# Kernel optimization log

Measured on AMD Instinct MI355X. Metric: run time of the kernel, lower is better.

Reference implementation:

```python
import jax, jax.numpy as jnp
import numpy as np

D_MODEL = 1024
N_HEADS = 16
D_HEAD = D_MODEL // N_HEADS
EPS = 1e-6


def _phi(x):
    # elu(x) + 1, guaranteed non-negative kernel feature map
    return jax.nn.elu(x) + 1.0


def setup_inputs() -> dict:
    key = jax.random.key(0)
    k1, k2, k3 = jax.random.split(key, 3)
    x = jax.random.normal(k1, (4, 4096, D_MODEL), dtype=jnp.float32)
    # torch nn.Linear weights: (out_features, in_features), y = x @ W.T
    s = 1.0 / np.sqrt(D_MODEL)
    w_qkv = jax.random.uniform(k2, (3 * D_MODEL, D_MODEL), minval=-s, maxval=s, dtype=jnp.float32)
    w_out = jax.random.uniform(k3, (D_MODEL, D_MODEL), minval=-s, maxval=s, dtype=jnp.float32)
    return {"x": x, "w_qkv": w_qkv, "w_out": w_out}


def reference(x, w_qkv, w_out):
    B, L, D = x.shape
    H, dh = N_HEADS, D_HEAD
    qkv = jnp.einsum('bld,ed->ble', x, w_qkv)            # (B,L,3D)
    qkv = qkv.reshape(B, L, 3, H, dh).transpose(2, 0, 3, 1, 4)  # (3,B,H,L,dh)
    q, k, v = _phi(qkv[0]), _phi(qkv[1]), qkv[2]         # each (B,H,L,dh)

    # time-major for scan: (L,B,H,dh)
    qT = q.transpose(2, 0, 1, 3)
    kT = k.transpose(2, 0, 1, 3)
    vT = v.transpose(2, 0, 1, 3)

    S0 = jnp.zeros((B, H, dh, dh), dtype=x.dtype)
    z0 = jnp.zeros((B, H, dh), dtype=x.dtype)

    def step(carry, inp):
        S, z = carry
        q_t, k_t, v_t = inp
        S = S + k_t[..., :, None] * v_t[..., None, :]    # bhde outer product
        z = z + k_t
        num = jnp.einsum('bhde,bhd->bhe', S, q_t)
        den = jnp.maximum(jnp.sum(z * q_t, axis=-1, keepdims=True), EPS)
        return (S, z), num / den

    _, out = jax.lax.scan(step, (S0, z0), (qT, kT, vT))  # out: (L,B,H,dh)
    out = out.transpose(1, 0, 2, 3).reshape(B, L, D)     # (B,L,D)
    return jnp.einsum('bld,ed->ble', out, w_out)
```

## Files before the change

### kernel.cpp

```cpp
#include <hip/hip_runtime.h>
#include <hip/hip_bf16.h>
#include <math.h>

#define B_SZc    4
#define L_SEQc   4096
#define EPSc     1e-6f
#define CHUNKc   128
#define NCHUNKc  32

#define QKV_PER_B  4194304ull
#define ATT_PER_B  4194304ull
#define X_PER_B    4194304ull
#define S_PER_B    2097152ull
#define Z_PER_B    32768ull

typedef __attribute__((ext_vector_type(8))) short s16x8;
typedef __attribute__((ext_vector_type(4))) short s16x4;
typedef __attribute__((ext_vector_type(4))) float f32x4;

__device__ __forceinline__ float phi_f(float x) {
    return x > 0.0f ? x + 1.0f : expf(x);
}
__device__ __forceinline__ float bf2f(short h) {
    return __uint_as_float(((unsigned int)(unsigned short)h) << 16);
}
__device__ __forceinline__ short f2bf(float f) {
    unsigned int u = __float_as_uint(f);
    u = (u + 0x7FFFu + ((u >> 16) & 1u)) >> 16;
    return (short)u;
}

#define GLOAD16(ldsp, gp) \
    __builtin_amdgcn_global_load_lds((const __attribute__((address_space(1))) void*)(gp), \
                                     (__attribute__((address_space(3))) void*)(ldsp), 16, 0, 0)

__global__ __launch_bounds__(256)
void cvt_f32_bf16(const float* __restrict__ in, short* __restrict__ out, int n)
{
    int i = (blockIdx.x * 256 + threadIdx.x) * 4;
    const int stride = gridDim.x * 256 * 4;
    for (; i < n; i += stride) {
        float4 v = *(const float4*)(in + i);
        short4 o = {f2bf(v.x), f2bf(v.y), f2bf(v.z), f2bf(v.w)};
        *(short4*)(out + i) = o;
    }
}

template<int MODE>
__global__ __launch_bounds__(256)
void gemm_bf16(const short* __restrict__ A, const short* __restrict__ Bm,
               int M, int N, int K, float* __restrict__ C,
               short* __restrict__ qb, short* __restrict__ kb,
               short* __restrict__ kTb, short* __restrict__ vTb)
{
    __shared__ __align__(16) short lA[128 * 32];
    __shared__ __align__(16) short lB[128 * 32];

    const int tid = threadIdx.x;
    const int lane = tid & 63;
    const int wave = tid >> 6;
    const int wr = wave >> 1, wc = wave & 1;
    const int bm = blockIdx.y, bn = blockIdx.x;

    const short* Abase = A + (size_t)bm * 128 * K;
    const short* Bbase = Bm + (size_t)bn * 128 * K;

    f32x4 acc[4][4];
#pragma unroll
    for (int i = 0; i < 4; ++i)
#pragma unroll
        for (int j = 0; j < 4; ++j) acc[i][j] = (f32x4){0.f, 0.f, 0.f, 0.f};

    const int lr = lane & 15;
    const int lk = (lane >> 4) * 8;

    for (int k0 = 0; k0 < K; k0 += 32) {
#pragma unroll
        for (int c2 = 0; c2 < 2; ++c2) {
            const int idx = c2 * 256 + tid;
            const int row = idx >> 2;
            const int ks  = (idx & 3) * 8;
            GLOAD16(&lA[idx * 8], Abase + (size_t)row * K + k0 + ks);
            GLOAD16(&lB[idx * 8], Bbase + (size_t)row * K + k0 + ks);
        }
        __syncthreads();
        s16x8 af[4], bf[4];
#pragma unroll
        for (int m = 0; m < 4; ++m)
            af[m] = *(const s16x8*)&lA[(wr * 64 + m * 16 + lr) * 32 + lk];
#pragma unroll
        for (int n = 0; n < 4; ++n)
            bf[n] = *(const s16x8*)&lB[(wc * 64 + n * 16 + lr) * 32 + lk];
#pragma unroll
        for (int m = 0; m < 4; ++m)
#pragma unroll
            for (int n = 0; n < 4; ++n)
                acc[m][n] = __builtin_amdgcn_mfma_f32_16x16x32_bf16(af[m], bf[n], acc[m][n], 0, 0, 0);
        __syncthreads();
    }

    const int cr0 = (lane >> 4) * 4;
    if (MODE == 0) {
#pragma unroll
        for (int m = 0; m < 4; ++m)
#pragma unroll
            for (int n = 0; n < 4; ++n) {
                const int col = bn * 128 + wc * 64 + n * 16 + lr;
#pragma unroll
                for (int j = 0; j < 4; ++j) {
                    const int row = bm * 128 + wr * 64 + m * 16 + cr0 + j;
                    C[(size_t)row * N + col] = acc[m][n][j];
                }
            }
    } else {
#pragma unroll
        for (int m = 0; m < 4; ++m)
#pragma unroll
            for (int n = 0; n < 4; ++n) {
                const int col = bn * 128 + wc * 64 + n * 16 + lr;
                const int which = col >> 10;
                const int h = (col >> 6) & 15;
                const int d = col & 63;
                const int row0 = bm * 128 + wr * 64 + m * 16 + cr0;
                const int b = row0 >> 12;
                const int l0 = row0 & 4095;
                const size_t bh64 = (size_t)(b * 16 + h);
                if (which == 0) {
#pragma unroll
                    for (int j = 0; j < 4; ++j)
                        qb[(bh64 * 4096 + l0 + j) * 64 + d] = f2bf(phi_f(acc[m][n][j]));
                } else if (which == 1) {
                    s16x4 pk;
#pragma unroll
                    for (int j = 0; j < 4; ++j) {
                        short v = f2bf(phi_f(acc[m][n][j]));
                        kb[(bh64 * 4096 + l0 + j) * 64 + d] = v;
                        pk[j] = v;
                    }
                    *(s16x4*)(kTb + (bh64 * 64 + d) * 4096 + l0) = pk;
                } else {
                    s16x4 pv;
#pragma unroll
                    for (int j = 0; j < 4; ++j) pv[j] = f2bf(acc[m][n][j]);
                    *(s16x4*)(vTb + (bh64 * 64 + d) * 4096 + l0) = pv;
                }
            }
    }
}

__global__ __launch_bounds__(256)
void chunk_kv(const short* __restrict__ kTb, const short* __restrict__ vTb,
              float* __restrict__ ST, float* __restrict__ z)
{
    const int wave = threadIdx.x >> 6;
    const int lane = threadIdx.x & 63;
    const int c = blockIdx.x * 4 + wave;
    const int bh = blockIdx.y;
    const short* kT = kTb + (size_t)bh * 64 * 4096 + c * CHUNKc;
    const short* vT = vTb + (size_t)bh * 64 * 4096 + c * CHUNKc;
    const int lr = lane & 15;
    const int lk = (lane >> 4) * 8;

    f32x4 acc[4][4];
    f32x4 accz[4];
#pragma unroll
    for (int m = 0; m < 4; ++m) {
        accz[m] = (f32x4){0.f, 0.f, 0.f, 0.f};
#pragma unroll
        for (int n = 0; n < 4; ++n) acc[m][n] = (f32x4){0.f, 0.f, 0.f, 0.f};
    }
    s16x8 ones;
#pragma unroll
    for (int j = 0; j < 8; ++j) ones[j] = (short)0x3F80;

#pragma unroll
    for (int ks = 0; ks < 4; ++ks) {
        const int t0 = ks * 32 + lk;
        s16x8 a[4], b[4];
#pragma unroll
        for (int m = 0; m < 4; ++m)
            a[m] = *(const s16x8*)(vT + (size_t)(m * 16 + lr) * 4096 + t0);
#pragma unroll
        for (int n = 0; n < 4; ++n)
            b[n] = *(const s16x8*)(kT + (size_t)(n * 16 + lr) * 4096 + t0);
#pragma unroll
        for (int m = 0; m < 4; ++m)
#pragma unroll
            for (int n = 0; n < 4; ++n)
                acc[m][n] = __builtin_amdgcn_mfma_f32_16x16x32_bf16(a[m], b[n], acc[m][n], 0, 0, 0);
#pragma unroll
        for (int n = 0; n < 4; ++n)
            accz[n] = __builtin_amdgcn_mfma_f32_16x16x32_bf16(ones, b[n], accz[n], 0, 0, 0);
    }

    float* STc = ST + ((size_t)bh * NCHUNKc + c) * 4096;
    const int er0 = (lane >> 4) * 4;
#pragma unroll
    for (int m = 0; m < 4; ++m)
#pragma unroll
        for (int n = 0; n < 4; ++n)
#pragma unroll
            for (int j = 0; j < 4; ++j)
                STc[(m * 16 + er0 + j) * 64 + n * 16 + lr] = acc[m][n][j];
    if (lane < 16) {
        float* zc = z + ((size_t)bh * NCHUNKc + c) * 64;
#pragma unroll
        for (int n = 0; n < 4; ++n) zc[n * 16 + lane] = accz[n][0];
    }
}

__global__ __launch_bounds__(256)
void prefix_chunks(float* __restrict__ ST, float* __restrict__ z)
{
    const int sec = blockIdx.x, bh = blockIdx.y;
    const int tid = threadIdx.x;
    if (sec < 16) {
        float* base = ST + (size_t)bh * NCHUNKc * 4096 + sec * 256 + tid;
        float acc = 0.0f;
#pragma unroll
        for (int c = 0; c < NCHUNKc; ++c) {
            float t = base[(size_t)c * 4096];
            base[(size_t)c * 4096] = acc;
            acc += t;
        }
    } else if (tid < 64) {
        float* base = z + (size_t)bh * NCHUNKc * 64 + tid;
        float acc = 0.0f;
#pragma unroll
        for (int c = 0; c < NCHUNKc; ++c) {
            float t = base[c * 64];
            base[c * 64] = acc;
            acc += t;
        }
    }
}

__global__ __launch_bounds__(256)
void chunk_out(const short* __restrict__ qb, const short* __restrict__ kb,
               const short* __restrict__ vTb, const float* __restrict__ ST,
               const float* __restrict__ z, short* __restrict__ attb)
{
    const int c = blockIdx.x, bh = blockIdx.y;
    const int b = bh >> 4, h = bh & 15;
    const short* qc = qb + ((size_t)bh * L_SEQc + c * CHUNKc) * 64;
    const short* kc = kb + ((size_t)bh * L_SEQc + c * CHUNKc) * 64;
    const short* vT = vTb + (size_t)bh * 64 * 4096 + c * CHUNKc;
    const float* STp = ST + ((size_t)bh * NCHUNKc + c) * 4096;
    const float* zp  = z + ((size_t)bh * NCHUNKc + c) * 64;

    __shared__ float P[128][130];
    __shared__ float den_s[128];

    const int tid = threadIdx.x;
    const int lane = tid & 63;
    const int wave = tid >> 6;
    const int wr = wave >> 1, wc = wave & 1;
    const int lr = lane & 15;
    const int lg = lane >> 4;
    const int lk = lg * 8;
    const int cr0 = lg * 4;

    {
        f32x4 p[4][4];
#pragma unroll
        for (int m = 0; m < 4; ++m)
#pragma unroll
            for (int n = 0; n < 4; ++n) p[m][n] = (f32x4){0.f, 0.f, 0.f, 0.f};
#pragma unroll
        for (int ks = 0; ks < 2; ++ks) {
            s16x8 a[4], bfr[4];
#pragma unroll
            for (int m = 0; m < 4; ++m)
                a[m] = *(const s16x8*)(qc + (size_t)(wr * 64 + m * 16 + lr) * 64 + ks * 32 + lk);
#pragma unroll
            for (int n = 0; n < 4; ++n)
                bfr[n] = *(const s16x8*)(kc + (size_t)(wc * 64 + n * 16 + lr) * 64 + ks * 32 + lk);
#pragma unroll
            for (int m = 0; m < 4; ++m)
#pragma unroll
                for (int n = 0; n < 4; ++n)
                    p[m][n] = __builtin_amdgcn_mfma_f32_16x16x32_bf16(a[m], bfr[n], p[m][n], 0, 0, 0);
        }
#pragma unroll
        for (int m = 0; m < 4; ++m)
#pragma unroll
            for (int n = 0; n < 4; ++n) {
                const int cc = wc * 64 + n * 16 + lr;
#pragma unroll
                for (int j = 0; j < 4; ++j) {
                    const int r = wr * 64 + m * 16 + cr0 + j;
                    P[r][cc] = (cc <= r) ? p[m][n][j] : 0.0f;
                }
            }
    }
    __syncthreads();

    {
        const int r = tid >> 1;
        const int half = tid & 1;
        float s = 0.0f;
        const float* Pr = &P[r][half * 64];
#pragma unroll
        for (int t = 0; t < 64; t += 2) {
            float2 v2 = *(const float2*)&Pr[t];
            s += v2.x + v2.y;
        }
        const short* qr = qc + r * 64 + half * 32;
        const float* zh = zp + half * 32;
#pragma unroll
        for (int d0 = 0; d0 < 32; d0 += 8) {
            s16x8 qv = *(const s16x8*)(qr + d0);
#pragma unroll
            for (int j = 0; j < 8; ++j) s += bf2f(qv[j]) * zh[d0 + j];
        }
        s += __shfl_xor(s, 1);
        if (half == 0) den_s[r] = fmaxf(s, EPSc);
    }
    __syncthreads();

    f32x4 num[4][2];
#pragma unroll
    for (int m = 0; m < 4; ++m)
#pragma unroll
        for (int n = 0; n < 2; ++n) num[m][n] = (f32x4){0.f, 0.f, 0.f, 0.f};

#pragma unroll
    for (int ks = 0; ks < 4; ++ks) {
        const int t0 = ks * 32 + lk;
        s16x8 a[4];
#pragma unroll
        for (int m = 0; m < 4; ++m) {
            const float* pr = &P[wr * 64 + m * 16 + lr][t0];
            float2 f0 = *(const float2*)&pr[0];
            float2 f1 = *(const float2*)&pr[2];
            float2 f2 = *(const float2*)&pr[4];
            float2 f3 = *(const float2*)&pr[6];
            s16x8 av;
            av[0] = f2bf(f0.x); av[1] = f2bf(f0.y);
            av[2] = f2bf(f1.x); av[3] = f2bf(f1.y);
            av[4] = f2bf(f2.x); av[5] = f2bf(f2.y);
            av[6] = f2bf(f3.x); av[7] = f2bf(f3.y);
            a[m] = av;
        }
#pragma unroll
        for (int n = 0; n < 2; ++n) {
            s16x8 bv = *(const s16x8*)(vT + (size_t)(wc * 32 + n * 16 + lr) * 4096 + t0);
#pragma unroll
            for (int m = 0; m < 4; ++m)
                num[m][n] = __builtin_amdgcn_mfma_f32_16x16x32_bf16(a[m], bv, num[m][n], 0, 0, 0);
        }
    }

#pragma unroll
    for (int kk = 0; kk < 2; ++kk) {
        s16x8 qa[4];
#pragma unroll
        for (int m = 0; m < 4; ++m)
            qa[m] = *(const s16x8*)(qc + (size_t)(wr * 64 + m * 16 + lr) * 64 + kk * 32 + lk);
#pragma unroll
        for (int n = 0; n < 2; ++n) {
            const float* sp = STp + (size_t)(wc * 32 + n * 16 + lr) * 64 + kk * 32 + lk;
            float4 s0 = *(const float4*)sp;
            float4 s1 = *(const float4*)(sp + 4);
            float sv[8] = {s0.x, s0.y, s0.z, s0.w, s1.x, s1.y, s1.z, s1.w};
            s16x8 bhi, blo;
#pragma unroll
            for (int j = 0; j < 8; ++j) {
                short hi = f2bf(sv[j]);
                bhi[j] = hi;
                blo[j] = f2bf(sv[j] - bf2f(hi));
            }
#pragma unroll
            for (int m = 0; m < 4; ++m) {
                num[m][n] = __builtin_amdgcn_mfma_f32_16x16x32_bf16(qa[m], bhi, num[m][n], 0, 0, 0);
                num[m][n] = __builtin_amdgcn_mfma_f32_16x16x32_bf16(qa[m], blo, num[m][n], 0, 0, 0);
            }
        }
    }

#pragma unroll
    for (int m = 0; m < 4; ++m)
#pragma unroll
        for (int n = 0; n < 2; ++n) {
            const int e = wc * 32 + n * 16 + lr;
#pragma unroll
            for (int j = 0; j < 4; ++j) {
                const int r = wr * 64 + m * 16 + cr0 + j;
                const float inv = 1.0f / den_s[r];
                attb[((size_t)(b * 4096 + c * CHUNKc + r)) * 1024 + h * 64 + e] =
                    f2bf(num[m][n][j] * inv);
            }
        }
}

extern "C" void kernel_launch(void* const* d_in, const int* in_sizes, int n_in,
                              void* d_out, int out_size, void* d_ws, size_t ws_size,
                              hipStream_t stream) {
    const float* x     = (const float*)d_in[0];
    const float* w_qkv = (const float*)d_in[1];
    const float* w_out = (const float*)d_in[2];
    float* out = (float*)d_out;

    const size_t fixedB = 2ull * (3072 * 1024 + 1024 * 1024);
    const size_t perB   = 2ull * X_PER_B + 2ull * 5 * QKV_PER_B + 2ull * ATT_PER_B
                        + 4ull * S_PER_B + 4ull * Z_PER_B;
    const size_t perB_real = 2ull * X_PER_B + 2ull * 4 * QKV_PER_B + 2ull * ATT_PER_B
                           + 4ull * S_PER_B + 4ull * Z_PER_B;
    (void)perB;
    int Bp = 1;
    if (ws_size >= fixedB + 4 * perB_real + 65536) Bp = 4;
    else if (ws_size >= fixedB + 2 * perB_real + 65536) Bp = 2;

    char* p = (char*)d_ws;
    short* wqkvb = (short*)p; p += 2ull * 3072 * 1024;
    short* woutb = (short*)p; p += 2ull * 1024 * 1024;
    short* xb    = (short*)p; p += 2ull * X_PER_B * Bp;
    short* qb    = (short*)p; p += 2ull * QKV_PER_B * Bp;
    short* kb    = (short*)p; p += 2ull * QKV_PER_B * Bp;
    short* kTb   = (short*)p; p += 2ull * QKV_PER_B * Bp;
    short* vTb   = (short*)p; p += 2ull * QKV_PER_B * Bp;
    short* attb  = (short*)p; p += 2ull * ATT_PER_B * Bp;
    float* S     = (float*)p; p += 4ull * S_PER_B * Bp;
    float* z     = (float*)p;

    const int Mp = Bp * 4096;
    const int BHp = Bp * 16;

    cvt_f32_bf16<<<dim3(1024), 256, 0, stream>>>(w_qkv, wqkvb, 3072 * 1024);
    cvt_f32_bf16<<<dim3(512), 256, 0, stream>>>(w_out, woutb, 1024 * 1024);

    for (int b0 = 0; b0 < B_SZc; b0 += Bp) {
        const float* xp = x + (size_t)b0 * 4096 * 1024;

        cvt_f32_bf16<<<dim3(2048), 256, 0, stream>>>(xp, xb, Mp * 1024);

        dim3 g1(3072 / 128, Mp / 128);
        gemm_bf16<1><<<g1, 256, 0, stream>>>(xb, wqkvb, Mp, 3072, 1024, nullptr,
                                             qb, kb, kTb, vTb);

        chunk_kv<<<dim3(NCHUNKc / 4, BHp), 256, 0, stream>>>(kTb, vTb, S, z);

        prefix_chunks<<<dim3(17, BHp), 256, 0, stream>>>(S, z);

        chunk_out<<<dim3(NCHUNKc, BHp), 256, 0, stream>>>(qb, kb, vTb, S, z, attb);

        dim3 g3(1024 / 128, Mp / 128);
        gemm_bf16<0><<<g3, 256, 0, stream>>>(attb, woutb, Mp, 1024, 1024,
                                             out + (size_t)b0 * 4096 * 1024,
                                             nullptr, nullptr, nullptr, nullptr);
    }
}
```

Measured before the change: 440.7 us.

## Stage QKV GEMM epilogue through LDS for coalesced stores and swizzle block order

The MODE 1 epilogue of the QKV GEMM now stages each 128x32 accumulator slice into shared memory. It then writes q/k rows and kT/vT transposed rows as 16-byte vector stores, replacing the scattered 2-byte and 8-byte global stores. The block index is also remapped in groups of 8 so that neighbouring workgroups are spread across the grid, aiming for better L2/XCD locality. The cost is extra LDS traffic and barriers per slice, and the swizzle assumes the workgroup count is divisible by 8.

```diff
diff --git a/kernel.cpp b/kernel.cpp
--- a/kernel.cpp
+++ b/kernel.cpp
@@ -53,14 +53,20 @@
                short* __restrict__ qb, short* __restrict__ kb,
                short* __restrict__ kTb, short* __restrict__ vTb)
 {
-    __shared__ __align__(16) short lA[128 * 32];
-    __shared__ __align__(16) short lB[128 * 32];
+    __shared__ __align__(16) short smem[8192];
+    short* lA = smem;
+    short* lB = smem + 4096;
 
     const int tid = threadIdx.x;
     const int lane = tid & 63;
     const int wave = tid >> 6;
     const int wr = wave >> 1, wc = wave & 1;
-    const int bm = blockIdx.y, bn = blockIdx.x;
+
+    int flat = blockIdx.y * gridDim.x + blockIdx.x;
+    const int nwg = gridDim.x * gridDim.y;
+    flat = (flat & 7) * (nwg >> 3) + (flat >> 3);
+    const int bm = flat / gridDim.x;
+    const int bn = flat % gridDim.x;
 
     const short* Abase = A + (size_t)bm * 128 * K;
     const short* Bbase = Bm + (size_t)bn * 128 * K;
@@ -73,6 +79,7 @@
 
     const int lr = lane & 15;
     const int lk = (lane >> 4) * 8;
+    const int cr0 = (lane >> 4) * 4;
 
     for (int k0 = 0; k0 < K; k0 += 32) {
 #pragma unroll
@@ -99,7 +106,6 @@
         __syncthreads();
     }
 
-    const int cr0 = (lane >> 4) * 4;
     if (MODE == 0) {
 #pragma unroll
         for (int m = 0; m < 4; ++m)
@@ -113,38 +119,59 @@
                 }
             }
     } else {
-#pragma unroll
-        for (int m = 0; m < 4; ++m)
-#pragma unroll
-            for (int n = 0; n < 4; ++n) {
-                const int col = bn * 128 + wc * 64 + n * 16 + lr;
-                const int which = col >> 10;
-                const int h = (col >> 6) & 15;
-                const int d = col & 63;
-                const int row0 = bm * 128 + wr * 64 + m * 16 + cr0;
-                const int b = row0 >> 12;
-                const int l0 = row0 & 4095;
-                const size_t bh64 = (size_t)(b * 16 + h);
-                if (which == 0) {
-#pragma unroll
-                    for (int j = 0; j < 4; ++j)
-                        qb[(bh64 * 4096 + l0 + j) * 64 + d] = f2bf(phi_f(acc[m][n][j]));
-                } else if (which == 1) {
-                    s16x4 pk;
-#pragma unroll
-                    for (int j = 0; j < 4; ++j) {
-                        short v = f2bf(phi_f(acc[m][n][j]));
-                        kb[(bh64 * 4096 + l0 + j) * 64 + d] = v;
-                        pk[j] = v;
-                    }
-                    *(s16x4*)(kTb + (bh64 * 64 + d) * 4096 + l0) = pk;
-                } else {
-                    s16x4 pv;
-#pragma unroll
-                    for (int j = 0; j < 4; ++j) pv[j] = f2bf(acc[m][n][j]);
-                    *(s16x4*)(vTb + (bh64 * 64 + d) * 4096 + l0) = pv;
+        const int which = bn >> 3;
+        const int b = bm >> 5;
+        const int l_base = (bm & 31) * 128;
+        short (*eps)[33] = (short(*)[33])smem;
+
+        for (int g = 0; g < 4; ++g) {
+            __syncthreads();
+            if (wc == (g >> 1)) {
+                const int subn = (g & 1) * 2;
+#pragma unroll
+                for (int nn = 0; nn < 2; ++nn) {
+                    const int n = subn + nn;
+                    const int lc = nn * 16 + lr;
+#pragma unroll
+                    for (int m = 0; m < 4; ++m)
+#pragma unroll
+                        for (int j = 0; j < 4; ++j) {
+                            float v = acc[m][n][j];
+                            if (which < 2) v = phi_f(v);
+                            eps[wr * 64 + m * 16 + cr0 + j][lc] = f2bf(v);
+                        }
                 }
             }
+            __syncthreads();
+            const int gcol = bn * 128 + g * 32;
+            const int h = (gcol >> 6) & 15;
+            const int d_base = gcol & 63;
+            const size_t bh = (size_t)(b * 16 + h);
+            if (which < 2) {
+                short* dst0 = (which == 0) ? qb : kb;
+                const int r = tid >> 2, q4 = tid & 3;
+#pragma unroll
+                for (int it = 0; it < 2; ++it) {
+                    const int rr = r + it * 64;
+                    s16x8 vv;
+#pragma unroll
+                    for (int i = 0; i < 8; ++i) vv[i] = eps[rr][q4 * 8 + i];
+                    *(s16x8*)(dst0 + (bh * 4096 + l_base + rr) * 64 + d_base + q4 * 8) = vv;
+                }
+            }
+            if (which >= 1) {
+                short* dstT = (which == 1) ? kTb : vTb;
+                const int dl = tid >> 4, ls = tid & 15;
+#pragma unroll
+                for (int it = 0; it < 2; ++it) {
+                    const int dd = dl + it * 16;
+                    s16x8 vv;
+#pragma unroll
+                    for (int i = 0; i < 8; ++i) vv[i] = eps[ls * 8 + i][dd];
+                    *(s16x8*)(dstT + (bh * 64 + d_base + dd) * 4096 + l_base + ls * 8) = vv;
+                }
+            }
+        }
     }
 }
 
@@ -402,11 +429,8 @@
     float* out = (float*)d_out;
 
     const size_t fixedB = 2ull * (3072 * 1024 + 1024 * 1024);
-    const size_t perB   = 2ull * X_PER_B + 2ull * 5 * QKV_PER_B + 2ull * ATT_PER_B
-                        + 4ull * S_PER_B + 4ull * Z_PER_B;
     const size_t perB_real = 2ull * X_PER_B + 2ull * 4 * QKV_PER_B + 2ull * ATT_PER_B
                            + 4ull * S_PER_B + 4ull * Z_PER_B;
-    (void)perB;
     int Bp = 1;
     if (ws_size >= fixedB + 4 * perB_real + 65536) Bp = 4;
     else if (ws_size >= fixedB + 2 * perB_real + 65536) Bp = 2;
```

After: 482.9 us. 9.6% more time.
